# Kernel tuning notes

Measured on AMD Instinct MI355X. Metric: run time of the kernel, lower is better.

Reference implementation:

```python
import jax, jax.numpy as jnp
import numpy as np

N_TOKEN = 32000
N_LAYER = 6
N_HEAD = 16
D_MODEL = 1024
D_HEAD = 64
D_INNER = 4096
QLEN = 512
MEM_LEN = 512
BSZ = 8
HD = N_HEAD * D_HEAD
SCALE = 1.0 / float(np.sqrt(D_HEAD))
NEG = -1e30


def _layer_norm(x, g, b, eps=1e-5):
    mu = jnp.mean(x, axis=-1, keepdims=True)
    var = jnp.var(x, axis=-1, keepdims=True)
    return (x - mu) * jax.lax.rsqrt(var + eps) * g + b


def _rel_shift(x):
    # x: [qlen, klen, bsz, n_head] -- TXL relative-position shift
    q, k, b, n = x.shape
    zp = jnp.zeros((q, 1, b, n), x.dtype)
    xp = jnp.concatenate([zp, x], axis=1).reshape(k + 1, q, b, n)
    return xp[1:].reshape(q, k, b, n)


def setup_inputs():
    key = jax.random.key(0)
    ks = jax.random.split(key, 12)
    s = 0.02
    rn = lambda k, *sh: jax.random.normal(k, sh, jnp.float32) * s
    z = lambda *sh: jnp.zeros(sh, jnp.float32)
    o = lambda *sh: jnp.ones(sh, jnp.float32)
    return {
        "data": jax.random.randint(ks[0], (QLEN, BSZ), 0, N_TOKEN),
        "target": jax.random.randint(ks[1], (QLEN, BSZ), 0, N_TOKEN),
        "memory": jax.random.normal(ks[2], (N_LAYER, MEM_LEN, BSZ, D_MODEL), jnp.float32),
        "emb_W": rn(ks[3], N_TOKEN, D_MODEL),  # tied input embedding / softmax head
        "r_w_bias": rn(ks[4], N_HEAD, D_HEAD),
        "r_r_bias": rn(ks[5], N_HEAD, D_HEAD),
        "Wq": rn(ks[6], N_LAYER, D_MODEL, HD),
        "Wkv": rn(ks[7], N_LAYER, D_MODEL, 2 * HD),
        "Wr": rn(ks[8], N_LAYER, D_MODEL, HD),
        "Wo": rn(ks[9], N_LAYER, HD, D_MODEL),
        "W1": rn(ks[10], N_LAYER, D_MODEL, D_INNER),
        "b1": z(N_LAYER, D_INNER),
        "W2": rn(ks[11], N_LAYER, D_INNER, D_MODEL),
        "b2": z(N_LAYER, D_MODEL),
        "ln1_g": o(N_LAYER, D_MODEL),
        "ln1_b": z(N_LAYER, D_MODEL),
        "ln2_g": o(N_LAYER, D_MODEL),
        "ln2_b": z(N_LAYER, D_MODEL),
    }


def _model(data, target, memory, emb_W, r_w_bias, r_r_bias, Wq, Wkv, Wr, Wo,
           W1, b1, W2, b2, ln1_g, ln1_b, ln2_g, ln2_b):
    qlen, bsz = data.shape
    mem = jax.lax.stop_gradient(memory)  # TXL detaches memories
    mlen = mem.shape[1]
    klen = mlen + qlen

    word_emb = emb_W[data]  # [q, b, d]

    # sinusoidal relative positions klen-1 .. 0
    pos_seq = jnp.arange(klen - 1, -1, -1, dtype=word_emb.dtype)
    inv_freq = 1.0 / (10000.0 ** (jnp.arange(0, D_MODEL, 2, dtype=word_emb.dtype) / D_MODEL))
    sin_inp = pos_seq[:, None] * inv_freq[None, :]
    pos = jnp.concatenate([jnp.sin(sin_inp), jnp.cos(sin_inp)], axis=-1)  # [klen, d]

    # causal mask with memory: query i can attend keys j <= i + mlen
    mask = jnp.arange(klen)[None, :] > (jnp.arange(qlen)[:, None] + mlen)  # [q, k]

    core = word_emb
    hids = [core]
    for i in range(N_LAYER):
        x_mem = jnp.concatenate([mem[i], core], axis=0)  # [klen, b, d]
        q = (core @ Wq[i]).reshape(qlen, bsz, N_HEAD, D_HEAD)
        kv = x_mem @ Wkv[i]
        k, v = jnp.split(kv, 2, axis=-1)
        k = k.reshape(klen, bsz, N_HEAD, D_HEAD)
        v = v.reshape(klen, bsz, N_HEAD, D_HEAD)
        r_k = (pos @ Wr[i]).reshape(klen, N_HEAD, D_HEAD)

        AC = jnp.einsum('ibnd,jbnd->ijbn', q + r_w_bias, k)
        BD = _rel_shift(jnp.einsum('ibnd,jnd->ijbn', q + r_r_bias, r_k))
        score = (AC + BD) * SCALE
        score = jnp.where(mask[:, :, None, None], NEG, score)
        prob = jax.nn.softmax(score, axis=1)
        vec = jnp.einsum('ijbn,jbnd->ibnd', prob, v).reshape(qlen, bsz, HD)
        attn_out = vec @ Wo[i]
        core = _layer_norm(core + attn_out, ln1_g[i], ln1_b[i])
        ff = jax.nn.relu(core @ W1[i] + b1[i]) @ W2[i] + b2[i]
        core = _layer_norm(core + ff, ln2_g[i], ln2_b[i])
        hids.append(core)

    # adaptive softmax with cutoffs=[] == full tied softmax
    logits = core @ emb_W.T  # [q, b, V]
    logp = jax.nn.log_softmax(logits, axis=-1)
    loss = -jnp.take_along_axis(logp, target[..., None], axis=-1)[..., 0]  # [q, b]

    new_mems = jnp.stack([
        jnp.concatenate([mem[i], hids[i]], axis=0)[-MEM_LEN:] for i in range(N_LAYER)
    ])
    new_mems = jax.lax.stop_gradient(new_mems)
    return loss, new_mems


def reference(data, target, memory, emb_W, r_w_bias, r_r_bias, Wq, Wkv, Wr, Wo,
              W1, b1, W2, b2, ln1_g, ln1_b, ln2_g, ln2_b):
    return _model(data, target, memory, emb_W, r_w_bias, r_r_bias, Wq, Wkv, Wr, Wo,
                  W1, b1, W2, b2, ln1_g, ln1_b, ln2_g, ln2_b)
```

## Files before the change

kernel.cpp:

```cpp
#include <hip/hip_runtime.h>
#include <hip/hip_bf16.h>
#include <math.h>

#define QLEN   512
#define MLEN   512
#define KLEN   1024
#define BSZ    8
#define NH     16
#define DH     64
#define DM     1024
#define DI     4096
#define NTOK   32000
#define NROW   4096
#define XROW   8192
#define VTILES 500

typedef __hip_bfloat16 bf16;
typedef __attribute__((ext_vector_type(8))) short bf16x8;
typedef __attribute__((ext_vector_type(4))) float f32x4;

__device__ __forceinline__ unsigned short f2b(float x) {
    union { float f; unsigned u; } a; a.f = x;
    unsigned r = a.u + 0x7fffu + ((a.u >> 16) & 1u);
    return (unsigned short)(r >> 16);
}
__device__ __forceinline__ float b2f(unsigned short h) {
    union { unsigned u; float f; } a; a.u = ((unsigned)h) << 16;
    return a.f;
}

__device__ __forceinline__ void gload_lds16(const void* g, void* l) {
    __builtin_amdgcn_global_load_lds(
        (const __attribute__((address_space(1))) unsigned int*)g,
        (__attribute__((address_space(3))) unsigned int*)l, 16, 0, 0);
}

__device__ __forceinline__ void kloop64(const unsigned short* __restrict__ Ag, int lda,
                                        const unsigned short* __restrict__ Bg, int ldb,
                                        unsigned short* As, unsigned short* Bs,
                                        int wave, int lane, int wm, int wn,
                                        int k0, int k1, f32x4 acc[4][4]) {
    int quad = lane >> 4, l16 = lane & 15, asw = l16 & 7;
    unsigned short* Al = As + (wave * 32) * 64;
    unsigned short* Bl = Bs + (wave * 32) * 64;
    for (int kt = k0; kt < k1; kt += 64) {
        #pragma unroll
        for (int k = 0; k < 4; k++) {
            gload_lds16(Ag + kt + (size_t)(k * 8) * lda, Al + (k * 8) * 64);
            gload_lds16(Bg + kt + (size_t)(k * 8) * ldb, Bl + (k * 8) * 64);
        }
        __syncthreads();
        #pragma unroll
        for (int kk = 0; kk < 2; kk++) {
            bf16x8 af[4], bfr[4];
            #pragma unroll
            for (int mi = 0; mi < 4; mi++)
                af[mi] = *(const bf16x8*)&As[(wm + mi * 16 + l16) * 64
                                             + (((kk * 4 + quad) ^ asw) * 8)];
            #pragma unroll
            for (int ni = 0; ni < 4; ni++)
                bfr[ni] = *(const bf16x8*)&Bs[(wn + ni * 16 + l16) * 64
                                              + (((kk * 4 + quad) ^ asw) * 8)];
            #pragma unroll
            for (int mi = 0; mi < 4; mi++)
                #pragma unroll
                for (int ni = 0; ni < 4; ni++)
                    acc[mi][ni] = __builtin_amdgcn_mfma_f32_16x16x32_bf16(
                        af[mi], bfr[ni], acc[mi][ni], 0, 0, 0);
        }
        __syncthreads();
    }
}

__global__ __launch_bounds__(256) void posb_kernel(unsigned short* __restrict__ posb) {
    int j = blockIdx.x;
    int t = threadIdx.x;
    float p = (float)(1023 - j);
    #pragma unroll
    for (int u = 0; u < 4; u++) {
        int dcol = t + u * 256;
        int k = dcol & 511;
        float invf = expf(-((float)k) * (1.0f / 512.0f) * 9.210340371976184f);
        float a = p * invf;
        posb[j * DM + dcol] = f2b((dcol < 512) ? sinf(a) : cosf(a));
    }
}

__global__ __launch_bounds__(256) void gather_emb(const int* __restrict__ data,
                                                  const float* __restrict__ emb,
                                                  float* __restrict__ out,
                                                  unsigned short* __restrict__ outb) {
    int row = blockIdx.x;
    int t = threadIdx.x;
    int tok = data[row];
    float4 v = ((const float4*)(emb + (size_t)tok * DM))[t];
    ((float4*)(out + (size_t)row * DM))[t] = v;
    ushort4 o;
    o.x = f2b(v.x); o.y = f2b(v.y); o.z = f2b(v.z); o.w = f2b(v.w);
    ((ushort4*)(outb + (size_t)row * DM))[t] = o;
}

__global__ __launch_bounds__(256) void cast_bf16(const float* __restrict__ src,
                                                 unsigned short* __restrict__ dst, int n4) {
    int i = blockIdx.x * 256 + threadIdx.x;
    if (i < n4) {
        float4 v = ((const float4*)src)[i];
        ushort4 o;
        o.x = f2b(v.x); o.y = f2b(v.y); o.z = f2b(v.z); o.w = f2b(v.w);
        ((ushort4*)dst)[i] = o;
    }
}

__global__ __launch_bounds__(256) void castT3(const float* __restrict__ s0,
                                              unsigned short* __restrict__ d0, int K0, int N0,
                                              const float* __restrict__ s1,
                                              unsigned short* __restrict__ d1, int K1, int N1,
                                              const float* __restrict__ s2,
                                              unsigned short* __restrict__ d2, int K2, int N2) {
    int id = blockIdx.x;
    const float* src; unsigned short* dst; int K, N;
    int n0 = (N0 >> 5) * (K0 >> 5), n1 = (N1 >> 5) * (K1 >> 5);
    if (id < n0)           { src = s0; dst = d0; K = K0; N = N0; }
    else if (id < n0 + n1) { id -= n0; src = s1; dst = d1; K = K1; N = N1; }
    else                   { id -= n0 + n1; src = s2; dst = d2; K = K2; N = N2; }
    __shared__ float T[32][33];
    int t = threadIdx.x;
    int bx = id % (N >> 5), by = id / (N >> 5);
    int k0 = by * 32, nc0 = bx * 32;
    int r = t >> 3, c4 = (t & 7) * 4;
    float4 v = *(const float4*)(src + (size_t)(k0 + r) * N + nc0 + c4);
    T[r][c4 + 0] = v.x; T[r][c4 + 1] = v.y; T[r][c4 + 2] = v.z; T[r][c4 + 3] = v.w;
    __syncthreads();
    ushort4 o;
    o.x = f2b(T[c4 + 0][r]); o.y = f2b(T[c4 + 1][r]);
    o.z = f2b(T[c4 + 2][r]); o.w = f2b(T[c4 + 3][r]);
    *(ushort4*)(dst + (size_t)(nc0 + r) * K + k0 + c4) = o;
}

template <bool BIAS, bool RELU, bool OUTBF16, int SPLITK = 1>
__global__ __launch_bounds__(256) void gemm_bt(const unsigned short* __restrict__ A,
                                               const unsigned short* __restrict__ B,
                                               const float* __restrict__ bias,
                                               void* __restrict__ Cout,
                                               int M, int N, int K) {
    __shared__ unsigned short As[128 * 64];
    __shared__ unsigned short Bs[128 * 64];
    int t = threadIdx.x;
    int wave = t >> 6, lane = t & 63;
    int bm = blockIdx.y * 128, bn = blockIdx.x * 128;
    int wm = (wave >> 1) * 64, wn = (wave & 1) * 64;
    int quad = lane >> 4, l16 = lane & 15;

    f32x4 acc[4][4] = {};

    int srow = wave * 32 + (lane >> 3);
    int scol = ((lane & 7) ^ (srow & 7)) * 8;
    const unsigned short* Ag = A + (size_t)(bm + srow) * K + scol;
    const unsigned short* Bg = B + (size_t)(bn + srow) * K + scol;

    int kchunk = K / SPLITK;
    int k0 = (SPLITK > 1) ? blockIdx.z * kchunk : 0;
    kloop64(Ag, K, Bg, K, As, Bs, wave, lane, wm, wn, k0, k0 + kchunk, acc);

    float* Cf = (float*)Cout + ((SPLITK > 1) ? (size_t)blockIdx.z * M * N : (size_t)0);
    #pragma unroll
    for (int mi = 0; mi < 4; mi++) {
        #pragma unroll
        for (int ni = 0; ni < 4; ni++) {
            int c = bn + wn + ni * 16 + l16;
            float bv = BIAS ? bias[c] : 0.0f;
            #pragma unroll
            for (int reg = 0; reg < 4; reg++) {
                int r = bm + wm + mi * 16 + quad * 4 + reg;
                float x = acc[mi][ni][reg];
                if (BIAS) x += bv;
                if (RELU) x = fmaxf(x, 0.0f);
                if (OUTBF16) ((unsigned short*)Cout)[(size_t)r * N + c] = f2b(x);
                else         Cf[(size_t)r * N + c] = x;
            }
        }
    }
}

__global__ __launch_bounds__(256) void kqv_gemm(const unsigned short* __restrict__ A,
                                                const unsigned short* __restrict__ B,
                                                const float* __restrict__ rwb,
                                                const float* __restrict__ rrb,
                                                unsigned short* __restrict__ qw,
                                                unsigned short* __restrict__ qr,
                                                unsigned short* __restrict__ Kh,
                                                unsigned short* __restrict__ Vth) {
    int cls = blockIdx.x >> 3;
    if (cls == 0 && blockIdx.y < 32) return;
    __shared__ unsigned short As[128 * 64];
    __shared__ unsigned short Bs[128 * 64];
    const int K = 1024;
    int t = threadIdx.x;
    int wave = t >> 6, lane = t & 63;
    int bm = blockIdx.y * 128, bn = blockIdx.x * 128;
    int wm = (wave >> 1) * 64, wn = (wave & 1) * 64;
    int quad = lane >> 4, l16 = lane & 15;

    f32x4 acc[4][4] = {};

    int srow = wave * 32 + (lane >> 3);
    int scol = ((lane & 7) ^ (srow & 7)) * 8;
    const unsigned short* Ag = A + (size_t)(bm + srow) * K + scol;
    const unsigned short* Bg = B + (size_t)(bn + srow) * K + scol;
    kloop64(Ag, K, Bg, K, As, Bs, wave, lane, wm, wn, 0, K, acc);

    if (cls == 0) {
        #pragma unroll
        for (int ni = 0; ni < 4; ni++) {
            int c = bn + wn + ni * 16 + l16;
            float wv = rwb[c], rv = rrb[c];
            #pragma unroll
            for (int mi = 0; mi < 4; mi++) {
                #pragma unroll
                for (int reg = 0; reg < 4; reg++) {
                    int r = bm + wm + mi * 16 + quad * 4 + reg;
                    int row = r - 4096;
                    int i = row >> 3;
                    float x = acc[mi][ni][reg];
                    qr[(size_t)row * DM + c] = f2b(x + rv);
                    qw[(size_t)row * DM + (c & ~63) + ((c & 63) ^ ((i & 7) << 3))] = f2b(x + wv);
                }
            }
        }
    } else if (cls == 1) {
        #pragma unroll
        for (int ni = 0; ni < 4; ni++) {
            int cc = bn + wn + ni * 16 + l16 - 1024;
            int d = cc & 63, hb = cc >> 6;
            #pragma unroll
            for (int mi = 0; mi < 4; mi++) {
                #pragma unroll
                for (int reg = 0; reg < 4; reg++) {
                    int r = bm + wm + mi * 16 + quad * 4 + reg;
                    int j = r >> 3, nb = hb * 8 + (r & 7);
                    Kh[(size_t)nb * 65536 + (size_t)j * 64 + (d ^ ((j & 7) << 3))] =
                        f2b(acc[mi][ni][reg]);
                }
            }
        }
    } else {
        #pragma unroll
        for (int ni = 0; ni < 4; ni++) {
            int cc = bn + wn + ni * 16 + l16 - 2048;
            int d = cc & 63, hb = cc >> 6;
            #pragma unroll
            for (int mi = 0; mi < 4; mi++) {
                #pragma unroll
                for (int reg = 0; reg < 4; reg++) {
                    int r = bm + wm + mi * 16 + quad * 4 + reg;
                    int j = r >> 3, nb = hb * 8 + (r & 7);
                    Vth[(size_t)nb * 65536 + (size_t)d * 1024
                        + (j & ~127) + ((j & 127) ^ ((d & 7) << 3))] =
                        f2b(acc[mi][ni][reg]);
                }
            }
        }
    }
}

__global__ __launch_bounds__(256) void lse_gemm_mfma(const unsigned short* __restrict__ A,
                                                     const unsigned short* __restrict__ B,
                                                     float* __restrict__ pmax,
                                                     float* __restrict__ psum) {
    __shared__ unsigned short As[128 * 64];
    __shared__ unsigned short Bs[128 * 64];
    int t = threadIdx.x;
    int wave = t >> 6, lane = t & 63;
    int bm = blockIdx.x * 128, bn = blockIdx.y * 128;
    int wm = (wave >> 1) * 64, wn = (wave & 1) * 64;
    int quad = lane >> 4, l16 = lane & 15;
    const int K = 1024;

    f32x4 acc[4][4] = {};

    int srow = wave * 32 + (lane >> 3);
    int scol = ((lane & 7) ^ (srow & 7)) * 8;
    const unsigned short* Ag = A + (size_t)(bm + srow) * K + scol;
    const unsigned short* Bg = B + (size_t)(bn + srow) * K + scol;
    kloop64(Ag, K, Bg, K, As, Bs, wave, lane, wm, wn, 0, K, acc);

    int vt = blockIdx.y * 2 + (wave & 1);
    #pragma unroll
    for (int mi = 0; mi < 4; mi++) {
        #pragma unroll
        for (int reg = 0; reg < 4; reg++) {
            float m = -1e30f;
            #pragma unroll
            for (int ni = 0; ni < 4; ni++) m = fmaxf(m, acc[mi][ni][reg]);
            #pragma unroll
            for (int off = 1; off < 16; off <<= 1) m = fmaxf(m, __shfl_xor(m, off, 64));
            float s = 0.0f;
            #pragma unroll
            for (int ni = 0; ni < 4; ni++) s += __expf(acc[mi][ni][reg] - m);
            #pragma unroll
            for (int off = 1; off < 16; off <<= 1) s += __shfl_xor(s, off, 64);
            if (l16 == 0) {
                int r = bm + wm + mi * 16 + quad * 4 + reg;
                pmax[(size_t)r * VTILES + vt] = m;
                psum[(size_t)r * VTILES + vt] = s;
            }
        }
    }
}

__global__ __launch_bounds__(256) void bd_gemm(const unsigned short* __restrict__ A,
                                               const unsigned short* __restrict__ B,
                                               int ldb,
                                               unsigned short* __restrict__ Bt) {
    __shared__ unsigned short As[128 * 64];
    __shared__ unsigned short Bs[128 * 64];
    int t = threadIdx.x;
    int wave = t >> 6, lane = t & 63;
    int bm = blockIdx.y * 128, bn = blockIdx.x * 128, n = blockIdx.z;
    int wm = (wave >> 1) * 64, wn = (wave & 1) * 64;
    int quad = lane >> 4, l16 = lane & 15;
    f32x4 acc[4][4] = {};
    int srow = wave * 32 + (lane >> 3);
    int scol = ((lane & 7) ^ (srow & 7)) * 8;
    const unsigned short* Ag = A + (size_t)(bm + srow) * DM + n * 64 + scol;
    const unsigned short* Bg = B + (size_t)(bn + srow) * ldb + n * 64 + scol;
    kloop64(Ag, DM, Bg, ldb, As, Bs, wave, lane, wm, wn, 0, 64, acc);

    #pragma unroll
    for (int mi = 0; mi < 4; mi++) {
        #pragma unroll
        for (int reg = 0; reg < 4; reg++) {
            int r = bm + wm + mi * 16 + quad * 4 + reg;
            int i = r >> 3;
            size_t rowbase = ((size_t)n * 4096 + r) * 1024;
            int sw = (i & 7) << 3;
            #pragma unroll
            for (int ni = 0; ni < 4; ni++) {
                int p = bn + wn + ni * 16 + l16;
                int j = p + i - 511;
                if ((unsigned)j < 1024u)
                    Bt[rowbase + (j & ~127) + ((j & 127) ^ sw)] = f2b(acc[mi][ni][reg]);
            }
        }
    }
}

__global__ __launch_bounds__(256) void flash_attn(const unsigned short* __restrict__ qw_b,
                                                  const unsigned short* __restrict__ Kh,
                                                  const unsigned short* __restrict__ Vth,
                                                  const unsigned short* __restrict__ Bt,
                                                  unsigned short* __restrict__ vecb) {
    int qb = blockIdx.x, b = blockIdx.y, n = blockIdx.z;
    int i0 = qb * 64, nb = n * 8 + b;
    int t = threadIdx.x, wave = t >> 6, lane = t & 63;
    int quad = lane >> 4, l16 = lane & 15;
    int wm = wave * 16;
    __shared__ unsigned short Qw_s[64 * 64];
    __shared__ unsigned short K_s[128 * 64];
    __shared__ unsigned short Vt_s[64 * 128];
    __shared__ unsigned short BD_s[64 * 128];

    {
        const unsigned short* g = qw_b
            + (size_t)((i0 + wave * 16 + (lane >> 3)) * 8 + b) * DM + n * 64 + (lane & 7) * 8;
        unsigned short* l = Qw_s + (wave * 16) * 64;
        gload_lds16(g, l);
        gload_lds16(g + (size_t)64 * DM, l + 8 * 64);
    }

    f32x4 o[4] = {};
    float m_run[4] = { -1e30f, -1e30f, -1e30f, -1e30f };
    float l_run[4] = {};

    int nt = ((i0 + 575) >> 7) + 1;
    for (int jt = 0; jt < nt; jt++) {
        int j0 = jt * 128;
        __syncthreads();
        {
            const unsigned short* g = Kh + (size_t)nb * 65536
                + (size_t)(j0 + wave * 32 + (lane >> 3)) * 64 + (lane & 7) * 8;
            unsigned short* l = K_s + (wave * 32) * 64;
            #pragma unroll
            for (int k = 0; k < 4; k++)
                gload_lds16(g + (size_t)k * 512, l + k * 512);
        }
        {
            const unsigned short* g = Vth + (size_t)nb * 65536
                + (size_t)(wave * 16 + (lane >> 4)) * 1024 + j0 + (lane & 15) * 8;
            unsigned short* l = Vt_s + (wave * 16) * 128;
            #pragma unroll
            for (int k = 0; k < 4; k++)
                gload_lds16(g + (size_t)k * 4096, l + k * 512);
        }
        {
            const unsigned short* g = Bt
                + ((size_t)n * 4096 + (size_t)(i0 + wave * 16 + (lane >> 4)) * 8 + b) * 1024
                + j0 + (lane & 15) * 8;
            unsigned short* l = BD_s + (wave * 16) * 128;
            #pragma unroll
            for (int k = 0; k < 4; k++)
                gload_lds16(g + (size_t)k * 32768, l + k * 512);
        }
        __syncthreads();

        int arow = wm + l16;
        int asw = (arow & 7) << 3;
        bf16x8 aq0 = *(const bf16x8*)&Qw_s[arow * 64 + ((quad * 8) ^ asw)];
        bf16x8 aq1 = *(const bf16x8*)&Qw_s[arow * 64 + ((32 + quad * 8) ^ asw)];
        f32x4 s[8];
        #pragma unroll
        for (int ni = 0; ni < 8; ni++) {
            int krow = ni * 16 + l16;
            int ksw = (krow & 7) << 3;
            bf16x8 b0 = *(const bf16x8*)&K_s[krow * 64 + ((quad * 8) ^ ksw)];
            bf16x8 b1 = *(const bf16x8*)&K_s[krow * 64 + ((32 + quad * 8) ^ ksw)];
            f32x4 z = {};
            z = __builtin_amdgcn_mfma_f32_16x16x32_bf16(aq0, b0, z, 0, 0, 0);
            s[ni] = __builtin_amdgcn_mfma_f32_16x16x32_bf16(aq1, b1, z, 0, 0, 0);
        }

        bool last = (jt == nt - 1);
        #pragma unroll
        for (int reg = 0; reg < 4; reg++) {
            int rl = quad * 4 + reg;
            int rsw = (rl & 7) << 3;
            #pragma unroll
            for (int ni = 0; ni < 8; ni++) {
                int c = ni * 16 + l16;
                float bd = b2f(BD_s[(wm + rl) * 128 + (c ^ rsw)]);
                float v = (s[ni][reg] + bd) * 0.125f;
                if (last && (j0 + c > i0 + wm + rl + 512)) v = -1e30f;
                s[ni][reg] = v;
            }
        }

        #pragma unroll
        for (int reg = 0; reg < 4; reg++) {
            float tm = s[0][reg];
            #pragma unroll
            for (int ni = 1; ni < 8; ni++) tm = fmaxf(tm, s[ni][reg]);
            #pragma unroll
            for (int off = 1; off < 16; off <<= 1) tm = fmaxf(tm, __shfl_xor(tm, off, 64));
            float mn = fmaxf(m_run[reg], tm);
            float alpha = __expf(m_run[reg] - mn);
            m_run[reg] = mn;
            float ts = 0.f;
            #pragma unroll
            for (int ni = 0; ni < 8; ni++) {
                float p = __expf(s[ni][reg] - mn);
                s[ni][reg] = p;
                ts += p;
            }
            #pragma unroll
            for (int off = 1; off < 16; off <<= 1) ts += __shfl_xor(ts, off, 64);
            l_run[reg] = l_run[reg] * alpha + ts;
            #pragma unroll
            for (int di = 0; di < 4; di++) o[di][reg] *= alpha;
        }

        #pragma unroll
        for (int reg = 0; reg < 4; reg++) {
            int rl = quad * 4 + reg;
            int rsw = (rl & 7) << 3;
            #pragma unroll
            for (int ni = 0; ni < 8; ni++) {
                int c = ni * 16 + l16;
                BD_s[(wm + rl) * 128 + (c ^ rsw)] = f2b(s[ni][reg]);
            }
        }

        #pragma unroll
        for (int kk = 0; kk < 4; kk++) {
            int prow = wm + l16;
            bf16x8 ap = *(const bf16x8*)&BD_s[prow * 128 + ((kk * 32 + quad * 8) ^ ((prow & 7) << 3))];
            #pragma unroll
            for (int di = 0; di < 4; di++) {
                int vr = di * 16 + l16;
                bf16x8 bv = *(const bf16x8*)&Vt_s[vr * 128 + ((kk * 32 + quad * 8) ^ ((vr & 7) << 3))];
                o[di] = __builtin_amdgcn_mfma_f32_16x16x32_bf16(ap, bv, o[di], 0, 0, 0);
            }
        }
    }

    #pragma unroll
    for (int reg = 0; reg < 4; reg++) {
        float inv = 1.0f / l_run[reg];
        int r = i0 + wm + quad * 4 + reg;
        #pragma unroll
        for (int di = 0; di < 4; di++) {
            vecb[(size_t)(r * 8 + b) * 1024 + n * 64 + di * 16 + l16] = f2b(o[di][reg] * inv);
        }
    }
}

template <int P, bool BIAS>
__global__ __launch_bounds__(256) void add_lnp(const float* __restrict__ x,
                                               const float* __restrict__ p,
                                               const float* __restrict__ bias,
                                               const float* __restrict__ g,
                                               const float* __restrict__ bb,
                                               float* __restrict__ outf,
                                               unsigned short* __restrict__ outb) {
    const size_t S = (size_t)NROW * DM;
    int row = blockIdx.x;
    int t = threadIdx.x;
    __shared__ float rs[256], rq[256];
    float v[4];
    float s = 0.f, sq = 0.f;
    #pragma unroll
    for (int u = 0; u < 4; u++) {
        int c = t + u * 256;
        size_t idx = (size_t)row * DM + c;
        float val = x[idx];
        if (BIAS) val += bias[c];
        #pragma unroll
        for (int k = 0; k < P; k++) val += p[(size_t)k * S + idx];
        v[u] = val;
        s += val;
        sq += val * val;
    }
    rs[t] = s;
    rq[t] = sq;
    __syncthreads();
    for (int off = 128; off > 0; off >>= 1) {
        if (t < off) { rs[t] += rs[t + off]; rq[t] += rq[t + off]; }
        __syncthreads();
    }
    float mu = rs[0] * (1.0f / 1024.0f);
    float var = rq[0] * (1.0f / 1024.0f) - mu * mu;
    float rstd = rsqrtf(var + 1e-5f);
    #pragma unroll
    for (int u = 0; u < 4; u++) {
        int c = t + u * 256;
        size_t idx = (size_t)row * DM + c;
        float o = (v[u] - mu) * rstd * g[c] + bb[c];
        if (outf) outf[idx] = o;
        outb[idx] = f2b(o);
    }
}

__global__ __launch_bounds__(256) void tgt_logit_bf(const unsigned short* __restrict__ core,
                                                    const unsigned short* __restrict__ emb,
                                                    const int* __restrict__ target,
                                                    float* __restrict__ out) {
    int row = blockIdx.x;
    int t = threadIdx.x;
    __shared__ float red[256];
    int tok = target[row];
    const unsigned short* a = core + (size_t)row * DM;
    const unsigned short* e = emb + (size_t)tok * DM;
    float s = 0.f;
    #pragma unroll
    for (int u = 0; u < 4; u++) {
        int c = t + u * 256;
        s += b2f(a[c]) * b2f(e[c]);
    }
    red[t] = s;
    __syncthreads();
    for (int off = 128; off > 0; off >>= 1) {
        if (t < off) red[t] += red[t + off];
        __syncthreads();
    }
    if (t == 0) out[row] = red[0];
}

__global__ __launch_bounds__(256) void lse_reduce_kernel(const float* __restrict__ pmax,
                                                         const float* __restrict__ psum,
                                                         const float* __restrict__ ltgt,
                                                         float* __restrict__ loss) {
    int row = blockIdx.x;
    int t = threadIdx.x;
    __shared__ float red[256];
    float m = -1e30f;
    for (int u = t; u < VTILES; u += 256) m = fmaxf(m, pmax[(size_t)row * VTILES + u]);
    red[t] = m;
    __syncthreads();
    for (int off = 128; off > 0; off >>= 1) {
        if (t < off) red[t] = fmaxf(red[t], red[t + off]);
        __syncthreads();
    }
    float M = red[0];
    __syncthreads();
    float s = 0.f;
    for (int u = t; u < VTILES; u += 256)
        s += psum[(size_t)row * VTILES + u] * __expf(pmax[(size_t)row * VTILES + u] - M);
    red[t] = s;
    __syncthreads();
    for (int off = 128; off > 0; off >>= 1) {
        if (t < off) red[t] += red[t + off];
        __syncthreads();
    }
    if (t == 0) loss[row] = M + logf(red[0]) - ltgt[row];
}

extern "C" void kernel_launch(void* const* d_in, const int* in_sizes, int n_in,
                              void* d_out, int out_size, void* d_ws, size_t ws_size,
                              hipStream_t stream) {
    const int*   data   = (const int*)d_in[0];
    const int*   target = (const int*)d_in[1];
    const float* memory = (const float*)d_in[2];
    const float* embW   = (const float*)d_in[3];
    const float* rwb    = (const float*)d_in[4];
    const float* rrb    = (const float*)d_in[5];
    const float* Wq     = (const float*)d_in[6];
    const float* Wkv    = (const float*)d_in[7];
    const float* Wr     = (const float*)d_in[8];
    const float* Wo     = (const float*)d_in[9];
    const float* W1     = (const float*)d_in[10];
    const float* b1     = (const float*)d_in[11];
    const float* W2     = (const float*)d_in[12];
    const float* b2     = (const float*)d_in[13];
    const float* ln1g   = (const float*)d_in[14];
    const float* ln1b   = (const float*)d_in[15];
    const float* ln2g   = (const float*)d_in[16];
    const float* ln2b   = (const float*)d_in[17];

    float* out  = (float*)d_out;
    float* loss = out;
    float* hids = out + 4096;

    const size_t SZ_CORE = (size_t)NROW * DM;

    const size_t MB = 1024 * 1024;
    char* base = (char*)d_ws;
    unsigned short* posb   = (unsigned short*)(base);
    unsigned short* rkball = (unsigned short*)(base + 2 * MB);
    unsigned short* qw_b   = (unsigned short*)(base + 14 * MB);
    unsigned short* qr_b   = (unsigned short*)(base + 22 * MB);
    unsigned short* wTA    = (unsigned short*)(base + 30 * MB);
    unsigned short* vecb   = (unsigned short*)(base + 30 * MB);
    unsigned short* Kh     = (unsigned short*)(base + 38 * MB);
    unsigned short* Vth    = (unsigned short*)(base + 54 * MB);
    unsigned short* Bt     = (unsigned short*)(base + 70 * MB);
    unsigned short* memb   = (unsigned short*)(base + 70 * MB);
    unsigned short* cinb   = (unsigned short*)(base + 78 * MB);
    float*          cmid   = (float*)(base + 86 * MB);
    unsigned short* wrT    = (unsigned short*)(base + 86 * MB);
    unsigned short* W1T    = (unsigned short*)(base + 14 * MB);
    unsigned short* W2T    = (unsigned short*)(base + 22 * MB);
    unsigned short* WoT    = (unsigned short*)(base + 134 * MB);
    float*          wop    = (float*)(base + 38 * MB);
    unsigned short* h1b    = (unsigned short*)(base + 102 * MB);
    float*          w2p    = (float*)(base + 134 * MB);
    unsigned short* cmidb  = (unsigned short*)(base + 166 * MB);
    unsigned short* embWb  = (unsigned short*)(base + 86 * MB);
    float*          pmax   = (float*)(base + 152 * MB);
    float*          psum   = (float*)(base + 162 * MB);
    float*          ltgt   = (float*)(base + 172 * MB);
    unsigned short* corefnb = cinb;

    posb_kernel<<<KLEN, 256, 0, stream>>>(posb);
    gather_emb<<<NROW, 256, 0, stream>>>(data, embW, hids, cinb);

    castT3<<<3072, 256, 0, stream>>>(
        Wr,                      wrT,                      DM, DM,
        Wr + (size_t)1 * DM * DM, wrT + (size_t)1 * DM * DM, DM, DM,
        Wr + (size_t)2 * DM * DM, wrT + (size_t)2 * DM * DM, DM, DM);
    castT3<<<3072, 256, 0, stream>>>(
        Wr + (size_t)3 * DM * DM, wrT + (size_t)3 * DM * DM, DM, DM,
        Wr + (size_t)4 * DM * DM, wrT + (size_t)4 * DM * DM, DM, DM,
        Wr + (size_t)5 * DM * DM, wrT + (size_t)5 * DM * DM, DM, DM);
    gemm_bt<false, false, true><<<dim3(48, 8), 256, 0, stream>>>(
        posb, wrT, nullptr, rkball, KLEN, 6 * DM, DM);

    for (int L = 0; L < 6; L++) {
        const float* cin = hids + (size_t)L * SZ_CORE;
        float* coutf = (L < 5) ? (hids + (size_t)(L + 1) * SZ_CORE) : nullptr;

        cast_bf16<<<4096, 256, 0, stream>>>(memory + (size_t)L * SZ_CORE, memb, 1 << 20);

        castT3<<<3072, 256, 0, stream>>>(
            Wq + (size_t)L * DM * DM,      wTA,                    DM, DM,
            Wkv + (size_t)L * DM * 2 * DM, wTA + (size_t)DM * DM,  DM, 2 * DM,
            Wq, wTA, 32, 32);

        kqv_gemm<<<dim3(24, 64), 256, 0, stream>>>(
            memb, wTA, rwb, rrb, qw_b, qr_b, Kh, Vth);

        bd_gemm<<<dim3(8, 32, 16), 256, 0, stream>>>(qr_b, rkball + (size_t)L * DM, 6 * DM, Bt);
        flash_attn<<<dim3(8, 8, 16), 256, 0, stream>>>(qw_b, Kh, Vth, Bt, vecb);

        castT3<<<9216, 256, 0, stream>>>(
            Wo + (size_t)L * DM * DM, WoT, DM, DM,
            W1 + (size_t)L * DM * DI, W1T, DM, DI,
            W2 + (size_t)L * DI * DM, W2T, DI, DM);

        gemm_bt<false, false, false, 2><<<dim3(8, 32, 2), 256, 0, stream>>>(
            vecb, WoT, nullptr, wop, NROW, DM, DM);

        add_lnp<2, false><<<NROW, 256, 0, stream>>>(
            cin, wop, nullptr, ln1g + L * DM, ln1b + L * DM, cmid, cmidb);

        gemm_bt<true, true, true><<<dim3(32, 32), 256, 0, stream>>>(
            cmidb, W1T, b1 + (size_t)L * DI, h1b, NROW, DI, DM);

        gemm_bt<false, false, false, 2><<<dim3(8, 32, 2), 256, 0, stream>>>(
            h1b, W2T, nullptr, w2p, NROW, DM, DI);

        add_lnp<2, true><<<NROW, 256, 0, stream>>>(
            cmid, w2p, b2 + (size_t)L * DM, ln2g + L * DM, ln2b + L * DM, coutf, cinb);
    }

    cast_bf16<<<32768, 256, 0, stream>>>(embW, embWb, (NTOK * DM) / 4);
    tgt_logit_bf<<<NROW, 256, 0, stream>>>(corefnb, embWb, target, ltgt);
    lse_gemm_mfma<<<dim3(32, 250), 256, 0, stream>>>(corefnb, embWb, pmax, psum);
    lse_reduce_kernel<<<NROW, 256, 0, stream>>>(pmax, psum, ltgt, loss);
}
```

Measured before the change: 3.192 ms.

## Prefetch next K/V/BD tile in registers in flash attention; compact kqv grid

```diff
diff --git a/kernel.cpp b/kernel.cpp
--- a/kernel.cpp
+++ b/kernel.cpp
@@ -190,14 +190,17 @@
                                                 unsigned short* __restrict__ qr,
                                                 unsigned short* __restrict__ Kh,
                                                 unsigned short* __restrict__ Vth) {
-    int cls = blockIdx.x >> 3;
-    if (cls == 0 && blockIdx.y < 32) return;
+    int id = blockIdx.x;
+    int cls, e, by;
+    if (id < 512)       { cls = 1; e = id & 7; by = id >> 3; }
+    else if (id < 1024) { id -= 512;  cls = 2; e = id & 7; by = id >> 3; }
+    else                { id -= 1024; cls = 0; e = id & 7; by = 32 + (id >> 3); }
     __shared__ unsigned short As[128 * 64];
     __shared__ unsigned short Bs[128 * 64];
     const int K = 1024;
     int t = threadIdx.x;
     int wave = t >> 6, lane = t & 63;
-    int bm = blockIdx.y * 128, bn = blockIdx.x * 128;
+    int bm = by * 128, bn = (cls * 8 + e) * 128;
     int wm = (wave >> 1) * 64, wn = (wave & 1) * 64;
     int quad = lane >> 4, l16 = lane & 15;
 
@@ -360,6 +363,17 @@
     __shared__ unsigned short Vt_s[64 * 128];
     __shared__ unsigned short BD_s[64 * 128];
 
+    const unsigned short* gK = Kh + (size_t)nb * 65536
+        + (size_t)(wave * 32 + (lane >> 3)) * 64 + (lane & 7) * 8;
+    const unsigned short* gV = Vth + (size_t)nb * 65536
+        + (size_t)(wave * 16 + (lane >> 4)) * 1024 + (lane & 15) * 8;
+    const unsigned short* gB = Bt
+        + ((size_t)n * 4096 + (size_t)(i0 + wave * 16 + (lane >> 4)) * 8 + b) * 1024
+        + (lane & 15) * 8;
+    unsigned short* lK = K_s + wave * 2048;
+    unsigned short* lV = Vt_s + wave * 2048;
+    unsigned short* lB = BD_s + wave * 2048;
+
     {
         const unsigned short* g = qw_b
             + (size_t)((i0 + wave * 16 + (lane >> 3)) * 8 + b) * DM + n * 64 + (lane & 7) * 8;
@@ -367,6 +381,12 @@
         gload_lds16(g, l);
         gload_lds16(g + (size_t)64 * DM, l + 8 * 64);
     }
+    #pragma unroll
+    for (int k = 0; k < 4; k++) {
+        gload_lds16(gK + (size_t)k * 512,   lK + k * 512);
+        gload_lds16(gV + (size_t)k * 4096,  lV + k * 512);
+        gload_lds16(gB + (size_t)k * 32768, lB + k * 512);
+    }
 
     f32x4 o[4] = {};
     float m_run[4] = { -1e30f, -1e30f, -1e30f, -1e30f };
@@ -376,38 +396,25 @@
     for (int jt = 0; jt < nt; jt++) {
         int j0 = jt * 128;
         __syncthreads();
-        {
-            const unsigned short* g = Kh + (size_t)nb * 65536
-                + (size_t)(j0 + wave * 32 + (lane >> 3)) * 64 + (lane & 7) * 8;
-            unsigned short* l = K_s + (wave * 32) * 64;
-            #pragma unroll
-            for (int k = 0; k < 4; k++)
-                gload_lds16(g + (size_t)k * 512, l + k * 512);
-        }
-        {
-            const unsigned short* g = Vth + (size_t)nb * 65536
-                + (size_t)(wave * 16 + (lane >> 4)) * 1024 + j0 + (lane & 15) * 8;
-            unsigned short* l = Vt_s + (wave * 16) * 128;
-            #pragma unroll
-            for (int k = 0; k < 4; k++)
-                gload_lds16(g + (size_t)k * 4096, l + k * 512);
-        }
-        {
-            const unsigned short* g = Bt
-                + ((size_t)n * 4096 + (size_t)(i0 + wave * 16 + (lane >> 4)) * 8 + b) * 1024
-                + j0 + (lane & 15) * 8;
-            unsigned short* l = BD_s + (wave * 16) * 128;
-            #pragma unroll
-            for (int k = 0; k < 4; k++)
-                gload_lds16(g + (size_t)k * 32768, l + k * 512);
-        }
-        __syncthreads();
+
+        float4 pk[4], pv[4], pb[4];
+        bool pf = (jt + 1 < nt);
+        if (pf) {
+            int j1 = j0 + 128;
+            #pragma unroll
+            for (int k = 0; k < 4; k++) {
+                pk[k] = *(const float4*)(gK + (size_t)j1 * 64 + (size_t)k * 512);
+                pv[k] = *(const float4*)(gV + j1 + (size_t)k * 4096);
+                pb[k] = *(const float4*)(gB + j1 + (size_t)k * 32768);
+            }
+        }
 
         int arow = wm + l16;
         int asw = (arow & 7) << 3;
         bf16x8 aq0 = *(const bf16x8*)&Qw_s[arow * 64 + ((quad * 8) ^ asw)];
         bf16x8 aq1 = *(const bf16x8*)&Qw_s[arow * 64 + ((32 + quad * 8) ^ asw)];
         f32x4 s[8];
+        __builtin_amdgcn_s_setprio(1);
         #pragma unroll
         for (int ni = 0; ni < 8; ni++) {
             int krow = ni * 16 + l16;
@@ -418,6 +425,7 @@
             z = __builtin_amdgcn_mfma_f32_16x16x32_bf16(aq0, b0, z, 0, 0, 0);
             s[ni] = __builtin_amdgcn_mfma_f32_16x16x32_bf16(aq1, b1, z, 0, 0, 0);
         }
+        __builtin_amdgcn_s_setprio(0);
 
         bool last = (jt == nt - 1);
         #pragma unroll
@@ -469,6 +477,7 @@
             }
         }
 
+        __builtin_amdgcn_s_setprio(1);
         #pragma unroll
         for (int kk = 0; kk < 4; kk++) {
             int prow = wm + l16;
@@ -478,6 +487,17 @@
                 int vr = di * 16 + l16;
                 bf16x8 bv = *(const bf16x8*)&Vt_s[vr * 128 + ((kk * 32 + quad * 8) ^ ((vr & 7) << 3))];
                 o[di] = __builtin_amdgcn_mfma_f32_16x16x32_bf16(ap, bv, o[di], 0, 0, 0);
+            }
+        }
+        __builtin_amdgcn_s_setprio(0);
+
+        __syncthreads();
+        if (pf) {
+            #pragma unroll
+            for (int k = 0; k < 4; k++) {
+                *(float4*)(lK + k * 512 + lane * 8) = pk[k];
+                *(float4*)(lV + k * 512 + lane * 8) = pv[k];
+                *(float4*)(lB + k * 512 + lane * 8) = pb[k];
             }
         }
     }
@@ -674,7 +694,7 @@
             Wkv + (size_t)L * DM * 2 * DM, wTA + (size_t)DM * DM,  DM, 2 * DM,
             Wq, wTA, 32, 32);
 
-        kqv_gemm<<<dim3(24, 64), 256, 0, stream>>>(
+        kqv_gemm<<<1280, 256, 0, stream>>>(
             memb, wTA, rwb, rrb, qw_b, qr_b, Kh, Vth);
 
         bd_gemm<<<dim3(8, 32, 16), 256, 0, stream>>>(qr_b, rkball + (size_t)L * DM, 6 * DM, Bt);
```

Measured after the change: 3.438 ms. 1.08x slower.
